# Kernel optimization log

Hardware: AMD Instinct MI355X
Metric: run time of the kernel (lower is better)

## Reference

```python
import jax, jax.numpy as jnp
import numpy as np

TOPK = 13
ALPHA = 1.0
BETA = 6.0
NUM_CLASSES = 80
NUM_ANCHORS = 100000
NUM_GT = 512
EPS = 1e-9


def _make_boxes(key, n):
    k1, k2 = jax.random.split(key)
    lt = jax.random.uniform(k1, (n, 2)) * 0.5          # x1, y1 in [0, 0.5)
    wh = jax.random.uniform(k2, (n, 2)) * 0.5 + 1e-3   # positive width/height
    return jnp.concatenate([lt, lt + wh], axis=-1)      # [n, 4] valid xyxy


def setup_inputs() -> dict:
    key = jax.random.key(0)
    k1, k2, k3, k4 = jax.random.split(key, 4)
    pd_scores = jax.random.uniform(k1, (NUM_ANCHORS, NUM_CLASSES), dtype=jnp.float32)
    pd_bboxes = _make_boxes(k2, NUM_ANCHORS)
    gt_labels = jax.random.randint(k3, (NUM_GT, 1), 0, NUM_CLASSES, dtype=jnp.int64)
    gt_bboxes = _make_boxes(k4, NUM_GT)
    return {"pd_scores": pd_scores, "pd_bboxes": pd_bboxes,
            "gt_labels": gt_labels, "gt_bboxes": gt_bboxes}


def box_iou(a, b):
    # a: [G, 4], b: [A, 4] in xyxy -> iou [G, A]
    lt = jnp.maximum(a[:, None, :2], b[None, :, :2])
    rb = jnp.minimum(a[:, None, 2:], b[None, :, 2:])
    wh = jnp.clip(rb - lt, 0.0)
    inter = wh[..., 0] * wh[..., 1]                      # [G, A]
    area_a = (a[:, 2] - a[:, 0]) * (a[:, 3] - a[:, 1])   # [G]
    area_b = (b[:, 2] - b[:, 0]) * (b[:, 3] - b[:, 1])   # [A]
    union = area_a[:, None] + area_b[None, :] - inter
    return inter / (union + EPS)


def select_topk_candidates(metrics, topk):
    # metrics: [G, A] -> bool mask [G, A] of per-row topk entries
    _, topk_idx = jax.lax.top_k(metrics, topk)           # [G, topk]
    rows = jnp.arange(metrics.shape[0])[:, None]
    mask = jnp.zeros(metrics.shape, dtype=bool)
    return mask.at[rows, topk_idx].set(True)


def reference(pd_scores, pd_bboxes, gt_labels, gt_bboxes):
    labels = gt_labels.reshape(-1)                       # [G]
    ious = box_iou(gt_bboxes, pd_bboxes)                 # [G, A]
    scores = pd_scores[:, labels].T                      # [G, A] gather by gt class
    metrics = (scores ** ALPHA) * (ious ** BETA)         # alignment metric [G, A]
    is_in_topk = select_topk_candidates(metrics, TOPK)   # [G, A] bool
    max_metrics = jnp.max(metrics, axis=0)               # [A]
    max_indices = jnp.argmax(metrics, axis=0)            # [A]
    target_labels = labels[max_indices]                  # [A]
    target_labels = jnp.where(max_metrics <= 0, NUM_CLASSES, target_labels)
    target_bboxes = gt_bboxes[max_indices]               # [A, 4]
    # is_in_topk is computed (as in the original) and returned so the topk/scatter
    return target_labels, target_bboxes, max_metrics, is_in_topk
```

## Files before the change

kernel.cpp:

```cpp
#include <hip/hip_runtime.h>
#include <cfloat>
#include <cstdint>

#define AN 100000
#define GN 512
#define NC 80
#define KK 13

#define CHUNKS 8
#define CH_LEN 12544
#define DUMP 16
#define GSLICE 4
#define GPS (GN / GSLICE)

typedef unsigned long long ull;

__device__ __forceinline__ float metric_f(
    float gx1, float gy1, float gx2, float gy2, float ga,
    float px1, float py1, float px2, float py2, float pa,
    float score)
{
    float ltx = fmaxf(gx1, px1), lty = fmaxf(gy1, py1);
    float rbx = fminf(gx2, px2), rby = fminf(gy2, py2);
    float w = fmaxf(rbx - ltx, 0.0f), h = fmaxf(rby - lty, 0.0f);
    float inter = w * h;
    float uni = ga + pa - inter;
    float iou = inter / (uni + 1e-9f);
    float i2 = iou * iou;
    float i6 = i2 * i2 * i2;
    return score * i6;
}

__device__ __forceinline__ float metric2(float4 g, float ga, float4 p, float sc)
{
    float pa = (p.z - p.x) * (p.w - p.y);
    return metric_f(g.x, g.y, g.z, g.w, ga, p.x, p.y, p.z, p.w, pa, sc);
}

__device__ __forceinline__ unsigned f2ord(float f)
{
    unsigned b = __float_as_uint(f);
    return b ^ (unsigned)(((int)b >> 31) | 0x80000000);
}
__device__ __forceinline__ float ord2f(unsigned u)
{
    unsigned b = (u & 0x80000000u) ? (u ^ 0x80000000u) : ~u;
    return __uint_as_float(b);
}

__device__ __forceinline__ void csw(float& va, int& ia, float& vb, int& ib)
{
    bool sw = (va < vb) || (va == vb && ia > ib);
    float tv = sw ? vb : va; int ti = sw ? ib : ia;
    vb = sw ? va : vb; ib = sw ? ia : ib;
    va = tv; ia = ti;
}

__device__ __forceinline__ void wsync()
{
    __builtin_amdgcn_sched_barrier(0);
    asm volatile("s_waitcnt lgkmcnt(0)" ::: "memory");
    __builtin_amdgcn_sched_barrier(0);
}

__device__ float flush_x(int lane, int n, const float* cand_v, const int* cand_i,
                         float& inc_v, int& inc_i)
{
    wsync();
    float v[8]; int ix[8];
    #pragma unroll
    for (int k = 0; k < 8; ++k) {
        int j = lane + (k << 6);
        bool ok = j < n;
        v[k]  = ok ? cand_v[j] : -FLT_MAX;
        ix[k] = ok ? cand_i[j] : 0x7fffffff;
    }
    csw(v[0],ix[0],v[1],ix[1]); csw(v[2],ix[2],v[3],ix[3]);
    csw(v[4],ix[4],v[5],ix[5]); csw(v[6],ix[6],v[7],ix[7]);
    csw(v[0],ix[0],v[2],ix[2]); csw(v[1],ix[1],v[3],ix[3]);
    csw(v[4],ix[4],v[6],ix[6]); csw(v[5],ix[5],v[7],ix[7]);
    csw(v[1],ix[1],v[2],ix[2]); csw(v[5],ix[5],v[6],ix[6]);
    csw(v[0],ix[0],v[4],ix[4]); csw(v[1],ix[1],v[5],ix[5]);
    csw(v[2],ix[2],v[6],ix[6]); csw(v[3],ix[3],v[7],ix[7]);
    csw(v[2],ix[2],v[4],ix[4]); csw(v[3],ix[3],v[5],ix[5]);
    csw(v[1],ix[1],v[2],ix[2]); csw(v[3],ix[3],v[4],ix[4]);
    csw(v[5],ix[5],v[6],ix[6]);
    bool c[8];
    #pragma unroll
    for (int j = 0; j < 8; ++j)
        c[j] = (v[j] > inc_v) || (v[j] == inc_v && ix[j] < inc_i);
    float h[9]; int hi[9];
    h[0] = c[0] ? v[0] : inc_v;  hi[0] = c[0] ? ix[0] : inc_i;
    #pragma unroll
    for (int j = 1; j < 8; ++j) {
        h[j]  = c[j] ? v[j]  : (c[j-1] ? inc_v : v[j-1]);
        hi[j] = c[j] ? ix[j] : (c[j-1] ? inc_i : ix[j-1]);
    }
    h[8] = c[7] ? inc_v : v[7];  hi[8] = c[7] ? inc_i : ix[7];

    float th = -FLT_MAX;
    #pragma unroll
    for (int r = 0; r < KK; ++r) {
        ull myp = ((ull)f2ord(h[0]) << 32) | (unsigned)(~hi[0]);
        ull p = myp;
        #pragma unroll
        for (int o = 32; o >= 1; o >>= 1) {
            ull q = __shfl_xor(p, o);
            p = p > q ? p : q;
        }
        float wv = ord2f((unsigned)(p >> 32));
        int   wi = (int)~((unsigned)p);
        if (lane == r) { inc_v = wv; inc_i = wi; }
        bool pop = (myp == p);
        #pragma unroll
        for (int j = 0; j < 8; ++j) {
            h[j]  = pop ? h[j+1]  : h[j];
            hi[j] = pop ? hi[j+1] : hi[j];
        }
        h[8]  = pop ? -FLT_MAX   : h[8];
        hi[8] = pop ? 0x7fffffff : hi[8];
        th = wv;
    }
    return th;
}

__device__ __forceinline__ void insert13(float* v, int* ix, float m, int a)
{
    bool worse = (m < v[KK - 1]) || (m == v[KK - 1] && a > ix[KK - 1]);
    if (worse) return;
    int p = 0;
    #pragma unroll
    for (int j = 0; j < KK; ++j)
        p += ((v[j] > m) || (v[j] == m && ix[j] < a)) ? 1 : 0;
    #pragma unroll
    for (int j = KK - 1; j >= 1; --j) {
        bool sh = (j > p);
        v[j]  = sh ? v[j - 1]  : v[j];
        ix[j] = sh ? ix[j - 1] : ix[j];
    }
    #pragma unroll
    for (int j = 0; j < KK; ++j) if (j == p) { v[j] = m; ix[j] = a; }
}

__global__ __launch_bounds__(256) void transpose_scores(
    const float* __restrict__ ps, float* __restrict__ scT)
{
    __shared__ float tile[64][NC + 1];
    int a0 = blockIdx.x * 64;
    int tid = threadIdx.x;
    for (int i = tid; i < 64 * NC / 4; i += 256) {
        int fi = i * 4;
        int a = fi / NC, c = fi % NC;
        if (a0 + a < AN) {
            float4 v = *reinterpret_cast<const float4*>(ps + (size_t)(a0 + a) * NC + c);
            tile[a][c] = v.x; tile[a][c + 1] = v.y; tile[a][c + 2] = v.z; tile[a][c + 3] = v.w;
        }
    }
    __syncthreads();
    int j = tid & 63, cg = tid >> 6;
    int a = a0 + j;
    if (a < AN) {
        for (int c = cg; c < NC; c += 4)
            scT[(size_t)c * AN + a] = tile[j][c];
    }
}

__global__ __launch_bounds__(256) void argmax_part(
    const float* __restrict__ pd_bboxes,
    const int*   __restrict__ gt_labels,
    const float* __restrict__ gt_bboxes,
    const float* __restrict__ scT,
    ull* __restrict__ part)
{
    __shared__ float4 gb[GPS];
    __shared__ float  ga[GPS];
    __shared__ int    glb[GPS];
    int slice = blockIdx.x & (GSLICE - 1);
    int ab = (blockIdx.x >> 2) * 256;
    int tid = threadIdx.x;
    int g0 = slice * GPS;
    for (int i = tid; i < GPS; i += 256) {
        float4 bb = ((const float4*)gt_bboxes)[g0 + i];
        gb[i] = bb;
        ga[i] = (bb.z - bb.x) * (bb.w - bb.y);
        glb[i] = gt_labels[g0 + i];
    }
    __syncthreads();
    int a = ab + tid;
    if (a >= AN) return;
    float4 pb = ((const float4*)pd_bboxes)[a];
    float pa = (pb.z - pb.x) * (pb.w - pb.y);
    float best = -1.0f; int bg = 0;
    for (int i = 0; i < GPS; ++i) {
        float sc = scT[(size_t)glb[i] * AN + a];
        float4 gx = gb[i];
        float m = metric_f(gx.x, gx.y, gx.z, gx.w, ga[i],
                           pb.x, pb.y, pb.z, pb.w, pa, sc);
        if (m > best) { best = m; bg = i; }
    }
    ull pack = ((ull)__float_as_uint(best) << 32) | (ull)(0xFFFFFFFFu - (unsigned)(g0 + bg));
    part[(size_t)slice * AN + a] = pack;
}

__global__ __launch_bounds__(256) void argmax_combine(
    const ull* __restrict__ part,
    const int* __restrict__ gt_labels,
    const float* __restrict__ gt_bboxes,
    float* __restrict__ out)
{
    int a = blockIdx.x * 256 + threadIdx.x;
    if (a >= AN) return;
    ull p0 = part[a], p1 = part[(size_t)AN + a];
    ull p2 = part[(size_t)2 * AN + a], p3 = part[(size_t)3 * AN + a];
    ull q0 = p0 > p1 ? p0 : p1;
    ull q1 = p2 > p3 ? p2 : p3;
    ull p = q0 > q1 ? q0 : q1;
    unsigned g = 0xFFFFFFFFu - (unsigned)(p & 0xFFFFFFFFull);
    float best = __uint_as_float((unsigned)(p >> 32));
    out[a] = (best <= 0.0f) ? (float)NC : (float)gt_labels[g];
    ((float4*)(out + AN))[a] = ((const float4*)gt_bboxes)[g];
    out[(size_t)5 * AN + a] = best;
}

template<bool FULL>
__device__ __forceinline__ void tile256(
    int tb, int aend, int lane, uint64_t lt,
    const float4* __restrict__ pd4, const float* __restrict__ srow,
    float4 b, float gax, float& th, int& cnt,
    float* cand_v, int* cand_i, float& inc_v, int& inc_i)
{
    int a0 = tb + lane, a1 = a0 + 64, a2 = a0 + 128, a3 = a0 + 192;
    int c0 = FULL ? a0 : min(a0, AN - 1);
    int c1 = FULL ? a1 : min(a1, AN - 1);
    int c2 = FULL ? a2 : min(a2, AN - 1);
    int c3 = FULL ? a3 : min(a3, AN - 1);
    float4 B0 = pd4[c0], B1 = pd4[c1], B2 = pd4[c2], B3 = pd4[c3];
    float s0 = srow[c0], s1 = srow[c1], s2 = srow[c2], s3 = srow[c3];
    float m0 = metric2(b, gax, B0, s0);
    float m1 = metric2(b, gax, B1, s1);
    float m2 = metric2(b, gax, B2, s2);
    float m3 = metric2(b, gax, B3, s3);
    bool h0 = (m0 > th) && (FULL || a0 < aend);
    bool h1 = (m1 > th) && (FULL || a1 < aend);
    bool h2 = (m2 > th) && (FULL || a2 < aend);
    bool h3 = (m3 > th) && (FULL || a3 < aend);
    if (__any(h0 | h1 | h2 | h3)) {
        uint64_t B;
        B = __ballot(h0);
        if (h0) { int p = cnt + __popcll(B & lt); cand_v[p] = m0; cand_i[p] = a0; }
        cnt += __popcll(B);
        B = __ballot(h1);
        if (h1) { int p = cnt + __popcll(B & lt); cand_v[p] = m1; cand_i[p] = a1; }
        cnt += __popcll(B);
        B = __ballot(h2);
        if (h2) { int p = cnt + __popcll(B & lt); cand_v[p] = m2; cand_i[p] = a2; }
        cnt += __popcll(B);
        B = __ballot(h3);
        if (h3) { int p = cnt + __popcll(B & lt); cand_v[p] = m3; cand_i[p] = a3; }
        cnt += __popcll(B);
        if (cnt >= 256) {
            th = flush_x(lane, cnt, cand_v, cand_i, inc_v, inc_i);
            cnt = 0;
        }
    }
}

__global__ __launch_bounds__(256, 4) void topk_pass1(
    const float* __restrict__ pd_bboxes,
    const int*   __restrict__ gt_labels,
    const float* __restrict__ gt_bboxes,
    const float* __restrict__ scT,
    float* __restrict__ out_v, int* __restrict__ out_i)
{
    __shared__ float cvA[4][512];
    __shared__ int   ciA[4][512];
    int w = threadIdx.x >> 6, lane = threadIdx.x & 63;
    float* cand_v = cvA[w]; int* cand_i = ciA[w];
    uint64_t lt = (1ull << lane) - 1ull;
    int gid = blockIdx.x * 4 + w;
    int g = gid & (GN - 1), c = gid >> 9;

    float4 b = ((const float4*)gt_bboxes)[g];
    float gax = (b.z - b.x) * (b.w - b.y);
    int lab = gt_labels[g];
    const float* srow = scT + (size_t)lab * AN;
    const float4* pd4 = (const float4*)pd_bboxes;

    int base = c * CH_LEN;
    int len = min(CH_LEN, AN - base);
    int nfull = len >> 8, rem = len & 255;
    int aend = base + len;

    float th = -FLT_MAX; int cnt = 0;
    float inc_v = -FLT_MAX; int inc_i = 0x7fffffff;

    for (int it = 0; it < nfull; ++it)
        tile256<true>(base + (it << 8), aend, lane, lt, pd4, srow,
                      b, gax, th, cnt, cand_v, cand_i, inc_v, inc_i);
    if (rem)
        tile256<false>(base + (nfull << 8), aend, lane, lt, pd4, srow,
                       b, gax, th, cnt, cand_v, cand_i, inc_v, inc_i);

    if (cnt > 0)
        flush_x(lane, cnt, cand_v, cand_i, inc_v, inc_i);

    if (lane < DUMP) {
        size_t o = ((size_t)g * CHUNKS + c) * DUMP + lane;
        out_v[o] = (lane < KK) ? inc_v : -FLT_MAX;
        out_i[o] = (lane < KK) ? inc_i : 0x7fffffff;
    }
}

__global__ __launch_bounds__(256) void topk_finalize(
    const float* __restrict__ in_v, const int* __restrict__ in_i,
    float* __restrict__ mask)
{
    int g = blockIdx.x, tid = threadIdx.x;
    float4* row4 = (float4*)(mask + (size_t)g * AN);
    float4 z = make_float4(0.f, 0.f, 0.f, 0.f);
    for (int j = tid; j < AN / 4; j += 256) row4[j] = z;
    __syncthreads();
    if (tid >= 64) return;
    int lane = tid;
    size_t rb = (size_t)g * (CHUNKS * DUMP);
    float v0 = in_v[rb + lane], v1 = in_v[rb + 64 + lane];
    int   i0 = in_i[rb + lane], i1 = in_i[rb + 64 + lane];
    csw(v0, i0, v1, i1);
    #pragma unroll
    for (int r = 0; r < KK; ++r) {
        ull myp = ((ull)f2ord(v0) << 32) | (unsigned)(~i0);
        ull p = myp;
        #pragma unroll
        for (int o = 32; o >= 1; o >>= 1) {
            ull q = __shfl_xor(p, o);
            p = p > q ? p : q;
        }
        int wi = (int)~((unsigned)p);
        if (lane == r) mask[(size_t)g * AN + wi] = 1.0f;
        bool pop = (myp == p);
        v0 = pop ? v1 : v0;          i0 = pop ? i1 : i0;
        v1 = pop ? -FLT_MAX : v1;    i1 = pop ? 0x7fffffff : i1;
    }
}

__global__ __launch_bounds__(256) void argmax_kernel(
    const float* __restrict__ pd_scores,
    const float* __restrict__ pd_bboxes,
    const int*   __restrict__ gt_labels,
    const float* __restrict__ gt_bboxes,
    const float* __restrict__ scT, int use_t,
    float* __restrict__ out)
{
    __shared__ float4 gb[GN];
    __shared__ float  ga[GN];
    __shared__ int    gl[GN];
    int tid = threadIdx.x;
    for (int g = tid; g < GN; g += 256) {
        float4 b = reinterpret_cast<const float4*>(gt_bboxes)[g];
        gb[g] = b;
        ga[g] = (b.z - b.x) * (b.w - b.y);
        gl[g] = gt_labels[g];
    }
    __syncthreads();
    int a = blockIdx.x * 256 + tid;
    if (a >= AN) return;
    float4 pb = reinterpret_cast<const float4*>(pd_bboxes)[a];
    float pa = (pb.z - pb.x) * (pb.w - pb.y);
    float best = -1.0f; int bg = 0;
    for (int g = 0; g < GN; ++g) {
        int lab = gl[g];
        float sc = use_t ? scT[(size_t)lab * AN + a] : pd_scores[(size_t)a * NC + lab];
        float4 gbx = gb[g];
        float m = metric_f(gbx.x, gbx.y, gbx.z, gbx.w, ga[g],
                           pb.x, pb.y, pb.z, pb.w, pa, sc);
        if (m > best) { best = m; bg = g; }
    }
    out[a] = (best <= 0.0f) ? (float)NC : (float)gl[bg];
    reinterpret_cast<float4*>(out + AN)[a] = gb[bg];
    out[5 * AN + a] = best;
}

__global__ __launch_bounds__(256) void topk_kernel_fallback(
    const float* __restrict__ pd_scores,
    const float* __restrict__ pd_bboxes,
    const int*   __restrict__ gt_labels,
    const float* __restrict__ gt_bboxes,
    const float* __restrict__ scT, int use_t,
    float* __restrict__ mask)
{
    __shared__ float sv[256 * KK];
    __shared__ int   si[256 * KK];
    int g = blockIdx.x, tid = threadIdx.x;
    float4 b = reinterpret_cast<const float4*>(gt_bboxes)[g];
    float gax = (b.z - b.x) * (b.w - b.y);
    int lab = gt_labels[g];
    float v[KK]; int idx[KK];
    #pragma unroll
    for (int j = 0; j < KK; ++j) { v[j] = -FLT_MAX; idx[j] = 0x7fffffff; }
    for (int a = tid; a < AN; a += 256) {
        float4 pb = reinterpret_cast<const float4*>(pd_bboxes)[a];
        float pa = (pb.z - pb.x) * (pb.w - pb.y);
        float sc = use_t ? scT[(size_t)lab * AN + a] : pd_scores[(size_t)a * NC + lab];
        float m = metric_f(b.x, b.y, b.z, b.w, gax, pb.x, pb.y, pb.z, pb.w, pa, sc);
        insert13(v, idx, m, a);
    }
    #pragma unroll
    for (int j = 0; j < KK; ++j) { sv[tid * KK + j] = v[j]; si[tid * KK + j] = idx[j]; }
    for (int off = 128; off >= 1; off >>= 1) {
        __syncthreads();
        if (tid < off) {
            int i = 0, jj = 0;
            float ov[KK]; int oi[KK];
            #pragma unroll
            for (int t = 0; t < KK; ++t) {
                float va = sv[tid * KK + i];          int ia = si[tid * KK + i];
                float vb = sv[(tid + off) * KK + jj]; int ib = si[(tid + off) * KK + jj];
                bool ta = (va > vb) || (va == vb && ia < ib);
                ov[t] = ta ? va : vb; oi[t] = ta ? ia : ib;
                i += ta ? 1 : 0; jj += ta ? 0 : 1;
            }
            #pragma unroll
            for (int t = 0; t < KK; ++t) { sv[tid * KK + t] = ov[t]; si[tid * KK + t] = oi[t]; }
        }
    }
    __syncthreads();
    if (tid < KK) mask[(size_t)g * AN + si[tid]] = 1.0f;
}

extern "C" void kernel_launch(void* const* d_in, const int* in_sizes, int n_in,
                              void* d_out, int out_size, void* d_ws, size_t ws_size,
                              hipStream_t stream)
{
    const float* pd_scores = (const float*)d_in[0];
    const float* pd_bboxes = (const float*)d_in[1];
    const int*   gt_labels = (const int*)d_in[2];
    const float* gt_bboxes = (const float*)d_in[3];
    float* out  = (float*)d_out;
    float* mask = out + (size_t)6 * AN;

    const size_t scT_b  = (size_t)NC * AN * sizeof(float);
    const size_t auxn   = (size_t)GN * CHUNKS * DUMP;
    const size_t aux_b  = auxn * 8;
    const size_t part_b = (size_t)GSLICE * AN * sizeof(ull);

    float* scT   = (float*)d_ws;
    float* aux_v = (float*)((char*)d_ws + scT_b);
    int*   aux_i = (int*)(aux_v + auxn);
    ull*   part  = (ull*)((char*)d_ws + scT_b + aux_b);

    if (ws_size >= scT_b + aux_b + part_b) {
        transpose_scores<<<(AN + 63) / 64, 256, 0, stream>>>(pd_scores, scT);
        topk_pass1<<<GN * CHUNKS / 4, 256, 0, stream>>>(
            pd_bboxes, gt_labels, gt_bboxes, scT, aux_v, aux_i);
        topk_finalize<<<GN, 256, 0, stream>>>(aux_v, aux_i, mask);
        argmax_part<<<((AN + 255) / 256) * GSLICE, 256, 0, stream>>>(
            pd_bboxes, gt_labels, gt_bboxes, scT, part);
        argmax_combine<<<(AN + 255) / 256, 256, 0, stream>>>(
            part, gt_labels, gt_bboxes, out);
    } else if (ws_size >= scT_b + aux_b) {
        transpose_scores<<<(AN + 63) / 64, 256, 0, stream>>>(pd_scores, scT);
        topk_pass1<<<GN * CHUNKS / 4, 256, 0, stream>>>(
            pd_bboxes, gt_labels, gt_bboxes, scT, aux_v, aux_i);
        topk_finalize<<<GN, 256, 0, stream>>>(aux_v, aux_i, mask);
        argmax_kernel<<<(AN + 255) / 256, 256, 0, stream>>>(
            pd_scores, pd_bboxes, gt_labels, gt_bboxes, scT, 1, out);
    } else if (ws_size >= scT_b) {
        hipMemsetAsync(mask, 0, (size_t)GN * AN * sizeof(float), stream);
        transpose_scores<<<(AN + 63) / 64, 256, 0, stream>>>(pd_scores, scT);
        argmax_kernel<<<(AN + 255) / 256, 256, 0, stream>>>(
            pd_scores, pd_bboxes, gt_labels, gt_bboxes, scT, 1, out);
        topk_kernel_fallback<<<GN, 256, 0, stream>>>(
            pd_scores, pd_bboxes, gt_labels, gt_bboxes, scT, 1, mask);
    } else {
        hipMemsetAsync(mask, 0, (size_t)GN * AN * sizeof(float), stream);
        argmax_kernel<<<(AN + 255) / 256, 256, 0, stream>>>(
            pd_scores, pd_bboxes, gt_labels, gt_bboxes, scT, 0, out);
        topk_kernel_fallback<<<GN, 256, 0, stream>>>(
            pd_scores, pd_bboxes, gt_labels, gt_bboxes, scT, 0, mask);
    }
}
```

Measured before the change: 183.9 us.

## Skip score loads when IoU alone cannot beat threshold; rebalance chunks and slices

Computes IoU^6 first in the topk and argmax paths and only loads the transposed score when IoU^6 exceeds the current threshold or best value. Scores lie in [0,1], so this prune is exact, and it is meant to cut memory traffic on the strided score rows. CHUNKS goes from 8 to 16 and GSLICE from 4 to 8, so topk_finalize merges four candidate lists per lane instead of two. argmax_part now handles two anchors per thread, and argmax_combine loops over the extra slices. The larger split adds more partial-result traffic and merge work in exchange for more parallelism.

Measured after the change: 213.7 us. 1.16x slower.

```diff
diff --git a/kernel.cpp b/kernel.cpp
--- a/kernel.cpp
+++ b/kernel.cpp
@@ -7,34 +7,25 @@
 #define NC 80
 #define KK 13
 
-#define CHUNKS 8
-#define CH_LEN 12544
+#define CHUNKS 16
+#define CH_LEN 6400
 #define DUMP 16
-#define GSLICE 4
+#define GSLICE 8
 #define GPS (GN / GSLICE)
 
 typedef unsigned long long ull;
 
-__device__ __forceinline__ float metric_f(
-    float gx1, float gy1, float gx2, float gy2, float ga,
-    float px1, float py1, float px2, float py2, float pa,
-    float score)
-{
-    float ltx = fmaxf(gx1, px1), lty = fmaxf(gy1, py1);
-    float rbx = fminf(gx2, px2), rby = fminf(gy2, py2);
+__device__ __forceinline__ float iou6_f(float4 g, float ga, float4 p)
+{
+    float pa = (p.z - p.x) * (p.w - p.y);
+    float ltx = fmaxf(g.x, p.x), lty = fmaxf(g.y, p.y);
+    float rbx = fminf(g.z, p.z), rby = fminf(g.w, p.w);
     float w = fmaxf(rbx - ltx, 0.0f), h = fmaxf(rby - lty, 0.0f);
     float inter = w * h;
     float uni = ga + pa - inter;
     float iou = inter / (uni + 1e-9f);
     float i2 = iou * iou;
-    float i6 = i2 * i2 * i2;
-    return score * i6;
-}
-
-__device__ __forceinline__ float metric2(float4 g, float ga, float4 p, float sc)
-{
-    float pa = (p.z - p.x) * (p.w - p.y);
-    return metric_f(g.x, g.y, g.z, g.w, ga, p.x, p.y, p.z, p.w, pa, sc);
+    return i2 * i2 * i2;
 }
 
 __device__ __forceinline__ unsigned f2ord(float f)
@@ -176,30 +167,43 @@
     __shared__ float  ga[GPS];
     __shared__ int    glb[GPS];
     int slice = blockIdx.x & (GSLICE - 1);
-    int ab = (blockIdx.x >> 2) * 256;
+    int ab = (blockIdx.x >> 3) * 512;
     int tid = threadIdx.x;
     int g0 = slice * GPS;
-    for (int i = tid; i < GPS; i += 256) {
-        float4 bb = ((const float4*)gt_bboxes)[g0 + i];
-        gb[i] = bb;
-        ga[i] = (bb.z - bb.x) * (bb.w - bb.y);
-        glb[i] = gt_labels[g0 + i];
+    if (tid < GPS) {
+        float4 bb = ((const float4*)gt_bboxes)[g0 + tid];
+        gb[tid] = bb;
+        ga[tid] = (bb.z - bb.x) * (bb.w - bb.y);
+        glb[tid] = gt_labels[g0 + tid];
     }
     __syncthreads();
-    int a = ab + tid;
-    if (a >= AN) return;
-    float4 pb = ((const float4*)pd_bboxes)[a];
-    float pa = (pb.z - pb.x) * (pb.w - pb.y);
-    float best = -1.0f; int bg = 0;
+    int aa = ab + tid, ab2 = ab + 256 + tid;
+    bool okA = aa < AN, okB = ab2 < AN;
+    int ca = okA ? aa : AN - 1, cb = okB ? ab2 : AN - 1;
+    float4 pba = ((const float4*)pd_bboxes)[ca];
+    float4 pbb = ((const float4*)pd_bboxes)[cb];
+    float bestA = -1.0f, bestB = -1.0f;
+    int bgA = 0, bgB = 0;
     for (int i = 0; i < GPS; ++i) {
-        float sc = scT[(size_t)glb[i] * AN + a];
         float4 gx = gb[i];
-        float m = metric_f(gx.x, gx.y, gx.z, gx.w, ga[i],
-                           pb.x, pb.y, pb.z, pb.w, pa, sc);
-        if (m > best) { best = m; bg = i; }
-    }
-    ull pack = ((ull)__float_as_uint(best) << 32) | (ull)(0xFFFFFFFFu - (unsigned)(g0 + bg));
-    part[(size_t)slice * AN + a] = pack;
+        float gax = ga[i];
+        int lab = glb[i];
+        const float* srow = scT + (size_t)lab * AN;
+        float i6a = iou6_f(gx, gax, pba);
+        float i6b = iou6_f(gx, gax, pbb);
+        float sa = (i6a > bestA) ? srow[ca] : 0.0f;
+        float sb = (i6b > bestB) ? srow[cb] : 0.0f;
+        float ma = sa * i6a;
+        float mb = sb * i6b;
+        if (ma > bestA) { bestA = ma; bgA = i; }
+        if (mb > bestB) { bestB = mb; bgB = i; }
+    }
+    if (okA)
+        part[(size_t)slice * AN + aa] =
+            ((ull)__float_as_uint(bestA) << 32) | (ull)(0xFFFFFFFFu - (unsigned)(g0 + bgA));
+    if (okB)
+        part[(size_t)slice * AN + ab2] =
+            ((ull)__float_as_uint(bestB) << 32) | (ull)(0xFFFFFFFFu - (unsigned)(g0 + bgB));
 }
 
 __global__ __launch_bounds__(256) void argmax_combine(
@@ -210,11 +214,12 @@
 {
     int a = blockIdx.x * 256 + threadIdx.x;
     if (a >= AN) return;
-    ull p0 = part[a], p1 = part[(size_t)AN + a];
-    ull p2 = part[(size_t)2 * AN + a], p3 = part[(size_t)3 * AN + a];
-    ull q0 = p0 > p1 ? p0 : p1;
-    ull q1 = p2 > p3 ? p2 : p3;
-    ull p = q0 > q1 ? q0 : q1;
+    ull p = part[a];
+    #pragma unroll
+    for (int s = 1; s < GSLICE; ++s) {
+        ull q = part[(size_t)s * AN + a];
+        p = p > q ? p : q;
+    }
     unsigned g = 0xFFFFFFFFu - (unsigned)(p & 0xFFFFFFFFull);
     float best = __uint_as_float((unsigned)(p >> 32));
     out[a] = (best <= 0.0f) ? (float)NC : (float)gt_labels[g];
@@ -235,16 +240,22 @@
     int c2 = FULL ? a2 : min(a2, AN - 1);
     int c3 = FULL ? a3 : min(a3, AN - 1);
     float4 B0 = pd4[c0], B1 = pd4[c1], B2 = pd4[c2], B3 = pd4[c3];
-    float s0 = srow[c0], s1 = srow[c1], s2 = srow[c2], s3 = srow[c3];
-    float m0 = metric2(b, gax, B0, s0);
-    float m1 = metric2(b, gax, B1, s1);
-    float m2 = metric2(b, gax, B2, s2);
-    float m3 = metric2(b, gax, B3, s3);
-    bool h0 = (m0 > th) && (FULL || a0 < aend);
-    bool h1 = (m1 > th) && (FULL || a1 < aend);
-    bool h2 = (m2 > th) && (FULL || a2 < aend);
-    bool h3 = (m3 > th) && (FULL || a3 < aend);
+    float i60 = iou6_f(b, gax, B0);
+    float i61 = iou6_f(b, gax, B1);
+    float i62 = iou6_f(b, gax, B2);
+    float i63 = iou6_f(b, gax, B3);
+    bool h0 = (i60 > th) && (FULL || a0 < aend);
+    bool h1 = (i61 > th) && (FULL || a1 < aend);
+    bool h2 = (i62 > th) && (FULL || a2 < aend);
+    bool h3 = (i63 > th) && (FULL || a3 < aend);
     if (__any(h0 | h1 | h2 | h3)) {
+        float s0 = h0 ? srow[c0] : 0.0f;
+        float s1 = h1 ? srow[c1] : 0.0f;
+        float s2 = h2 ? srow[c2] : 0.0f;
+        float s3 = h3 ? srow[c3] : 0.0f;
+        float m0 = s0 * i60, m1 = s1 * i61, m2 = s2 * i62, m3 = s3 * i63;
+        h0 = h0 && (m0 > th); h1 = h1 && (m1 > th);
+        h2 = h2 && (m2 > th); h3 = h3 && (m3 > th);
         uint64_t B;
         B = __ballot(h0);
         if (h0) { int p = cnt + __popcll(B & lt); cand_v[p] = m0; cand_i[p] = a0; }
@@ -323,9 +334,13 @@
     if (tid >= 64) return;
     int lane = tid;
     size_t rb = (size_t)g * (CHUNKS * DUMP);
-    float v0 = in_v[rb + lane], v1 = in_v[rb + 64 + lane];
-    int   i0 = in_i[rb + lane], i1 = in_i[rb + 64 + lane];
-    csw(v0, i0, v1, i1);
+    float v0 = in_v[rb + lane],       v1 = in_v[rb + 64 + lane];
+    float v2 = in_v[rb + 128 + lane], v3 = in_v[rb + 192 + lane];
+    int   i0 = in_i[rb + lane],       i1 = in_i[rb + 64 + lane];
+    int   i2 = in_i[rb + 128 + lane], i3 = in_i[rb + 192 + lane];
+    csw(v0, i0, v1, i1); csw(v2, i2, v3, i3);
+    csw(v0, i0, v2, i2); csw(v1, i1, v3, i3);
+    csw(v1, i1, v2, i2);
     #pragma unroll
     for (int r = 0; r < KK; ++r) {
         ull myp = ((ull)f2ord(v0) << 32) | (unsigned)(~i0);
@@ -338,8 +353,10 @@
         int wi = (int)~((unsigned)p);
         if (lane == r) mask[(size_t)g * AN + wi] = 1.0f;
         bool pop = (myp == p);
-        v0 = pop ? v1 : v0;          i0 = pop ? i1 : i0;
-        v1 = pop ? -FLT_MAX : v1;    i1 = pop ? 0x7fffffff : i1;
+        v0 = pop ? v1 : v0;  i0 = pop ? i1 : i0;
+        v1 = pop ? v2 : v1;  i1 = pop ? i2 : i1;
+        v2 = pop ? v3 : v2;  i2 = pop ? i3 : i2;
+        v3 = pop ? -FLT_MAX : v3;  i3 = pop ? 0x7fffffff : i3;
     }
 }
 
@@ -365,14 +382,11 @@
     int a = blockIdx.x * 256 + tid;
     if (a >= AN) return;
     float4 pb = reinterpret_cast<const float4*>(pd_bboxes)[a];
-    float pa = (pb.z - pb.x) * (pb.w - pb.y);
     float best = -1.0f; int bg = 0;
     for (int g = 0; g < GN; ++g) {
         int lab = gl[g];
         float sc = use_t ? scT[(size_t)lab * AN + a] : pd_scores[(size_t)a * NC + lab];
-        float4 gbx = gb[g];
-        float m = metric_f(gbx.x, gbx.y, gbx.z, gbx.w, ga[g],
-                           pb.x, pb.y, pb.z, pb.w, pa, sc);
+        float m = sc * iou6_f(gb[g], ga[g], pb);
         if (m > best) { best = m; bg = g; }
     }
     out[a] = (best <= 0.0f) ? (float)NC : (float)gl[bg];
@@ -399,9 +413,8 @@
     for (int j = 0; j < KK; ++j) { v[j] = -FLT_MAX; idx[j] = 0x7fffffff; }
     for (int a = tid; a < AN; a += 256) {
         float4 pb = reinterpret_cast<const float4*>(pd_bboxes)[a];
-        float pa = (pb.z - pb.x) * (pb.w - pb.y);
         float sc = use_t ? scT[(size_t)lab * AN + a] : pd_scores[(size_t)a * NC + lab];
-        float m = metric_f(b.x, b.y, b.z, b.w, gax, pb.x, pb.y, pb.z, pb.w, pa, sc);
+        float m = sc * iou6_f(b, gax, pb);
         insert13(v, idx, m, a);
     }
     #pragma unroll
@@ -453,7 +466,7 @@
         topk_pass1<<<GN * CHUNKS / 4, 256, 0, stream>>>(
             pd_bboxes, gt_labels, gt_bboxes, scT, aux_v, aux_i);
         topk_finalize<<<GN, 256, 0, stream>>>(aux_v, aux_i, mask);
-        argmax_part<<<((AN + 255) / 256) * GSLICE, 256, 0, stream>>>(
+        argmax_part<<<((AN + 511) / 512) * GSLICE, 256, 0, stream>>>(
             pd_bboxes, gt_labels, gt_bboxes, scT, part);
         argmax_combine<<<(AN + 255) / 256, 256, 0, stream>>>(
             part, gt_labels, gt_bboxes, out);
```
